# Performance work log

Measured on AMD Instinct MI355X. Metric: run time of the kernel, lower is better.

The kernel has to match this reference:

```python
import jax, jax.numpy as jnp
import numpy as np

B, S, D = 4, 2048, 1024
H, HD = 16, 64  # num_heads, head_dim
TD = H * HD     # total_dim
SCALE = HD ** -0.5


def setup_inputs() -> dict:
    key = jax.random.key(0)
    ks = jax.random.split(key, 9)
    std = 1.0 / np.sqrt(D)
    return {
        "x": jax.random.normal(ks[0], (B, S, D), dtype=jnp.float32),
        "Wq": jax.random.uniform(ks[1], (D, TD), jnp.float32, -std, std),
        "bq": jax.random.uniform(ks[2], (TD,), jnp.float32, -std, std),
        "Wk": jax.random.uniform(ks[3], (D, TD), jnp.float32, -std, std),
        "bk": jax.random.uniform(ks[4], (TD,), jnp.float32, -std, std),
        "Wv": jax.random.uniform(ks[5], (D, TD), jnp.float32, -std, std),
        "bv": jax.random.uniform(ks[6], (TD,), jnp.float32, -std, std),
        "Wo": jax.random.uniform(ks[7], (TD, D), jnp.float32, -std, std),
        "bo": jax.random.uniform(ks[8], (D,), jnp.float32, -std, std),
    }


def reference(x, Wq, bq, Wk, bk, Wv, bv, Wo, bo):
    # projections -> [B, H, S, HD]
    def split_heads(t):
        return t.reshape(B, S, H, HD).transpose(0, 2, 1, 3)

    q = split_heads(x @ Wq + bq)
    k = split_heads(x @ Wk + bk)
    v = split_heads(x @ Wv + bv)

    # attention scores [B, H, S, S]
    scores = jnp.einsum("bhqd,bhkd->bhqk", q, k) * SCALE
    weights = jax.nn.softmax(scores, axis=-1)
    # dropout is identity in eval mode (p effectively 0)
    attn = jnp.einsum("bhqk,bhkd->bhqd", weights, v)  # [B, H, S, HD]
    attn = attn.transpose(0, 2, 1, 3).reshape(B, S, TD)
    return attn @ Wo + bo
```

## Files before the change

### kernel.cpp

```cpp
#include <hip/hip_runtime.h>
#include <hip/hip_bf16.h>
#include <stdint.h>

#define B_ 4
#define S_ 2048
#define D_ 1024
#define H_ 16
#define HD_ 64
#define TD_ 1024

typedef __attribute__((ext_vector_type(4))) float f32x4;
typedef __attribute__((ext_vector_type(8))) __bf16 bf16x8;
typedef __attribute__((ext_vector_type(4))) __bf16 bf16x4;

__device__ __forceinline__ f32x4 mfma_16x16x32(bf16x8 a, bf16x8 b, f32x4 c) {
  return __builtin_amdgcn_mfma_f32_16x16x32_bf16(a, b, c, 0, 0, 0);
}

__device__ __forceinline__ float fexp2(float x) {
#if __has_builtin(__builtin_amdgcn_exp2f)
  return __builtin_amdgcn_exp2f(x);
#else
  return exp2f(x);
#endif
}

__device__ __forceinline__ uint32_t pkbf16(float lo, float hi) {
  uint32_t r;
  asm("v_cvt_pk_bf16_f32 %0, %1, %2" : "=v"(r) : "v"(lo), "v"(hi));
  return r;
}

__device__ __forceinline__ void gload16(const void* g, void* l) {
  __builtin_amdgcn_global_load_lds(
      (const __attribute__((address_space(1))) uint32_t*)(uintptr_t)g,
      (__attribute__((address_space(3))) uint32_t*)(uintptr_t)l,
      16, 0, 0);
}

__device__ __forceinline__ int xcd_swz(int flat, int nwg) {
  return (flat & 7) * (nwg >> 3) + (flat >> 3);
}


__global__ __launch_bounds__(256) void conv_x_kernel(const float* __restrict__ in,
                                                     __bf16* __restrict__ out) {
  size_t i = ((size_t)blockIdx.x * 256 + threadIdx.x) * 8;
  float4 a = *(const float4*)(in + i);
  float4 b = *(const float4*)(in + i + 4);
  bf16x8 o;
  o[0] = (__bf16)a.x; o[1] = (__bf16)a.y; o[2] = (__bf16)a.z; o[3] = (__bf16)a.w;
  o[4] = (__bf16)b.x; o[5] = (__bf16)b.y; o[6] = (__bf16)b.z; o[7] = (__bf16)b.w;
  *(bf16x8*)(out + i) = o;
}

__global__ __launch_bounds__(256) void wconv4_kernel(
    const float* __restrict__ w0, const float* __restrict__ w1,
    const float* __restrict__ w2, const float* __restrict__ w3,
    __bf16* __restrict__ o0, __bf16* __restrict__ o1,
    __bf16* __restrict__ o2, __bf16* __restrict__ o3, float scale0) {
  const float* in; __bf16* out; float scale;
  switch (blockIdx.z) {
    case 0: in = w0; out = o0; scale = scale0; break;
    case 1: in = w1; out = o1; scale = 1.0f; break;
    case 2: in = w2; out = o2; scale = 1.0f; break;
    default: in = w3; out = o3; scale = 1.0f; break;
  }
  __shared__ float t[64][65];
  const int bx = blockIdx.x * 64;
  const int by = blockIdx.y * 64;
  for (int e = threadIdx.x; e < 4096; e += 256) {
    int r = e >> 6, c = e & 63;
    t[r][c] = in[(size_t)(by + r) * 1024 + bx + c];
  }
  __syncthreads();
  for (int e = threadIdx.x; e < 4096; e += 256) {
    int r = e >> 6, c = e & 63;
    out[(size_t)(bx + r) * 1024 + by + c] = (__bf16)(t[c][r] * scale);
  }
}


#define STG3(SLOT)                                                      \
  gload16(srcA, dstA + (SLOT) * 8192);                                  \
  gload16(srcB, dstB + (SLOT) * 16384);                                 \
  gload16(srcB + 131072, dstB + (SLOT) * 16384 + 8192);                 \
  srcA += 32; srcB += 32;

#define COMPUTE_HALF(SLOT)                                              \
  {                                                                     \
    bf16x8 afr[4], bb[4];                                               \
    _Pragma("unroll") for (int mi = 0; mi < 4; ++mi)                    \
      afr[mi] = *(const bf16x8*)(aptr + (SLOT) * 8192 + mi * 1024);     \
    _Pragma("unroll") for (int ni = 0; ni < 4; ++ni)                    \
      bb[ni] = *(const bf16x8*)(bptr + (SLOT) * 16384 + ni * 1024);     \
    __builtin_amdgcn_s_setprio(1);                                      \
    _Pragma("unroll") for (int mi = 0; mi < 4; ++mi)                    \
      _Pragma("unroll") for (int ni = 0; ni < 4; ++ni)                  \
        acc[mi][ni] = mfma_16x16x32(afr[mi], bb[ni], acc[mi][ni]);      \
    __builtin_amdgcn_s_setprio(0);                                      \
  }

#define BAR_LGKM  asm volatile("s_waitcnt lgkmcnt(0)\n\ts_barrier" ::: "memory")
#define BAR_VM(N) asm volatile("s_waitcnt vmcnt(" #N ")\n\ts_barrier" ::: "memory")
#define BAR_VL(N) asm volatile("s_waitcnt vmcnt(" #N ") lgkmcnt(0)\n\ts_barrier" ::: "memory")

__global__ __launch_bounds__(512, 4) void gemm_qkv3(
    const __bf16* __restrict__ A, const __bf16* __restrict__ Bt,
    const float* __restrict__ bq, const float* __restrict__ bk,
    const float* __restrict__ bv, __bf16* __restrict__ Qout,
    __bf16* __restrict__ Kout, __bf16* __restrict__ Vout, float qscale) {
  __shared__ char SM[73728];
  const int tid = threadIdx.x, lane = tid & 63, wid = tid >> 6;
  const int lrow = lane & 15, g = lane >> 4;
  const int wm = wid >> 2, wn = wid & 3;
  const int flat = blockIdx.y * 12 + blockIdx.x;
  const int swz = xcd_swz(flat, 768);
  const int n0 = (swz % 12) * 256, m0 = (swz / 12) * 128;

  f32x4 acc[4][4];
  const f32x4 zero = {0.f, 0.f, 0.f, 0.f};
#pragma unroll
  for (int i = 0; i < 4; ++i)
#pragma unroll
    for (int j = 0; j < 4; ++j) acc[i][j] = zero;

  const int r0 = tid >> 2, c0 = tid & 3;
  const int csw = c0 ^ ((r0 >> 1) & 3);
  const __bf16* srcA = A + (size_t)(m0 + r0) * 1024 + csw * 8;
  const __bf16* srcB = Bt + (size_t)(n0 + r0) * 1024 + csw * 8;
  char* dstA = SM + wid * 1024;
  char* dstB = SM + 24576 + wid * 1024;

  const int sw = (lrow >> 1) & 3;
  const char* aptr = SM + (wm * 64 + lrow) * 64 + ((g ^ sw) << 4);
  const char* bptr = SM + 24576 + (wn * 64 + lrow) * 64 + ((g ^ sw) << 4);

  STG3(0)
  STG3(1)
  asm volatile("s_waitcnt vmcnt(3)\n\ts_barrier" ::: "memory");

  for (int it = 0; it < 10; ++it) {
    STG3(2)
    COMPUTE_HALF(0)
    BAR_VL(3);
    STG3(0)
    COMPUTE_HALF(1)
    BAR_VL(3);
    STG3(1)
    COMPUTE_HALF(2)
    BAR_VL(3);
  }
  COMPUTE_HALF(0)
  BAR_VL(0);
  COMPUTE_HALF(1)

  const int sel = n0 >> 10;
  if (sel < 2) {
    const float* bias = sel ? bk : bq;
    const float bsc = sel ? 1.0f : qscale;
    __bf16* Out = sel ? Kout : Qout;
#pragma unroll
    for (int mi = 0; mi < 4; ++mi) {
#pragma unroll
      for (int ni = 0; ni < 4; ++ni) {
        const int mbase = m0 + wm * 64 + mi * 16 + g * 4;
        const int nloc = (n0 & 1023) + wn * 64 + ni * 16 + lrow;
        const float bvc = bias[nloc] * bsc;
        const int h = nloc >> 6, hd = nloc & 63;
#pragma unroll
        for (int r = 0; r < 4; ++r) {
          const int m = mbase + r;
          const int b = m >> 11, s = m & 2047;
          Out[((size_t)(b * H_ + h) * S_ + s) * HD_ + hd] = (__bf16)(acc[mi][ni][r] + bvc);
        }
      }
    }
  } else {
#pragma unroll
    for (int mi = 0; mi < 4; ++mi) {
#pragma unroll
      for (int ni = 0; ni < 4; ++ni) {
        const int mbase = m0 + wm * 64 + mi * 16 + g * 4;
        const int t = (n0 & 1023) + wn * 64 + ni * 16 + lrow;
        const float bvc = bv[t];
        bf16x4 w;
#pragma unroll
        for (int r = 0; r < 4; ++r) w[r] = (__bf16)(acc[mi][ni][r] + bvc);
        *(bf16x4*)(Vout + (size_t)t * (B_ * S_) + mbase) = w;
      }
    }
  }
}


#define STG_O(SLOT, KOFF)                                               \
  gload16(srcA + (KOFF), dstA + (SLOT) * 8192);                         \
  gload16(srcA + 65536 + (KOFF), dstA + (SLOT) * 8192 + 4096);          \
  gload16(srcB + (KOFF), dstB + (SLOT) * 8192);                         \
  gload16(srcB + 65536 + (KOFF), dstB + (SLOT) * 8192 + 4096);

#define COMPUTE_O(SLOT)                                                 \
  {                                                                     \
    bf16x8 afr[4], bb[4];                                               \
    _Pragma("unroll") for (int mi = 0; mi < 4; ++mi)                    \
      afr[mi] = *(const bf16x8*)(aptr + (SLOT) * 8192 + mi * 1024);     \
    _Pragma("unroll") for (int ni = 0; ni < 4; ++ni)                    \
      bb[ni] = *(const bf16x8*)(bptr + (SLOT) * 8192 + ni * 1024);      \
    __builtin_amdgcn_s_setprio(1);                                      \
    _Pragma("unroll") for (int mi = 0; mi < 4; ++mi)                    \
      _Pragma("unroll") for (int ni = 0; ni < 4; ++ni)                  \
        acc[mi][ni] = mfma_16x16x32(afr[mi], bb[ni], acc[mi][ni]);      \
    __builtin_amdgcn_s_setprio(0);                                      \
  }

__global__ __launch_bounds__(256, 4) void gemm_out_ring(
    const __bf16* __restrict__ A, const __bf16* __restrict__ Bt,
    const float* __restrict__ bias, float* __restrict__ Cout) {
  __shared__ char SM[32768];
  const int tid = threadIdx.x, lane = tid & 63, wid = tid >> 6;
  const int lrow = lane & 15, g = lane >> 4;
  const int wm = wid >> 1, wn = wid & 1;
  const int flat = blockIdx.y * 8 + blockIdx.x;
  const int swz = xcd_swz(flat, 512);
  const int n0 = (swz & 7) * 128, m0 = (swz >> 3) * 128;

  f32x4 acc[4][4];
  const f32x4 zero = {0.f, 0.f, 0.f, 0.f};
#pragma unroll
  for (int i = 0; i < 4; ++i)
#pragma unroll
    for (int j = 0; j < 4; ++j) acc[i][j] = zero;

  const int r0 = tid >> 2, c0 = tid & 3;
  const int csw = c0 ^ ((r0 >> 1) & 3);
  const __bf16* srcA = A + (size_t)(m0 + r0) * 1024 + csw * 8;
  const __bf16* srcB = Bt + (size_t)(n0 + r0) * 1024 + csw * 8;
  char* dstA = SM + wid * 1024;
  char* dstB = SM + 16384 + wid * 1024;

  const int sw = (lrow >> 1) & 3;
  const char* aptr = SM + (wm * 64 + lrow) * 64 + ((g ^ sw) << 4);
  const char* bptr = SM + 16384 + (wn * 64 + lrow) * 64 + ((g ^ sw) << 4);

  STG_O(0, 0)
  STG_O(1, 32)
  srcA += 64; srcB += 64;
  BAR_VM(4);

  for (int it = 0; it < 15; ++it) {
    COMPUTE_O(0)
    BAR_LGKM;
    STG_O(0, 0)
    BAR_VM(4);
    COMPUTE_O(1)
    BAR_LGKM;
    STG_O(1, 32)
    BAR_VM(4);
    srcA += 64; srcB += 64;
  }
  COMPUTE_O(0)
  BAR_LGKM;
  BAR_VM(0);
  COMPUTE_O(1)

#pragma unroll
  for (int mi = 0; mi < 4; ++mi) {
#pragma unroll
    for (int ni = 0; ni < 4; ++ni) {
      const int mbase = m0 + wm * 64 + mi * 16 + g * 4;
      const int ncol = n0 + wn * 64 + ni * 16 + lrow;
      const float bvc = bias[ncol];
#pragma unroll
      for (int r = 0; r < 4; ++r)
        Cout[(size_t)(mbase + r) * 1024 + ncol] = acc[mi][ni][r] + bvc;
    }
  }
}


__global__ __launch_bounds__(256, 4) void attn_kernel(
    const __bf16* __restrict__ Q, const __bf16* __restrict__ Kp,
    const __bf16* __restrict__ VT, __bf16* __restrict__ O) {
  const int flat = blockIdx.y * gridDim.x + blockIdx.x;
  const int swz = (flat & 7) * 128 + (flat >> 3);
  const int bh = swz >> 4;
  const int q0 = (swz & 15) * 128;
  const int tid = threadIdx.x, lane = tid & 63, wid = tid >> 6;
  const int lrow = lane & 15, g = lane >> 4;
  const int s7 = lrow & 7;
  const int b = bh >> 4, h = bh & 15;

  const __bf16* Qb = Q + (size_t)bh * S_ * HD_;

  __shared__ char SMEM[32768];

  const int qrowA = q0 + wid * 32 + lrow;
  const int qrowB = qrowA + 16;
  const bf16x8 qf0a = *(const bf16x8*)(Qb + (size_t)qrowA * HD_ + g * 8);
  const bf16x8 qf1a = *(const bf16x8*)(Qb + (size_t)qrowA * HD_ + 32 + g * 8);
  const bf16x8 qf0b = *(const bf16x8*)(Qb + (size_t)qrowB * HD_ + g * 8);
  const bf16x8 qf1b = *(const bf16x8*)(Qb + (size_t)qrowB * HD_ + 32 + g * 8);

  bf16x8 ones;
#pragma unroll
  for (int i = 0; i < 8; ++i) ones[i] = (__bf16)1.0f;

  const int gi0 = wid * 64 + lane;
  const int row0 = gi0 >> 3, sg0 = gi0 & 7;
  const int kc0 = sg0 ^ (row0 & 7);
  const int kvoff = row0 * HD_ + kc0 * 8;
  const int vvoff = row0 * (B_ * S_) + kc0 * 8;
  const __bf16* Kt = Kp + (size_t)bh * S_ * HD_;
  const __bf16* Vt = VT + (size_t)(h * HD_) * (B_ * S_) + b * S_;
  char* kd0 = SMEM + wid * 1024;
  char* vd0 = SMEM + 16384 + wid * 1024;

  const char* addrA = SMEM + lrow * 128 + ((g ^ s7) << 4);
  const char* addrB = SMEM + lrow * 128 + (((4 + g) ^ s7) << 4);

  f32x4 laccA, laccB;
  f32x4 oaA[4], oaB[4];
  const f32x4 zero = {0.f, 0.f, 0.f, 0.f};
  const f32x4 minit = {-8.f, -8.f, -8.f, -8.f};
  laccA = zero; laccB = zero;
#pragma unroll
  for (int i = 0; i < 4; ++i) { oaA[i] = zero; oaB[i] = zero; }

  gload16(Kt + kvoff, kd0); gload16(Kt + 32 * HD_ + kvoff, kd0 + 4096);
  gload16(Vt + vvoff, vd0); gload16(Vt + (size_t)32 * (B_ * S_) + vvoff, vd0 + 4096);
  Kt += 64 * HD_; Vt += 64;
  __syncthreads();

  auto stage = [&](const int bo) {
    gload16(Kt + kvoff, kd0 + bo); gload16(Kt + 32 * HD_ + kvoff, kd0 + bo + 4096);
    gload16(Vt + vvoff, vd0 + bo);
    gload16(Vt + (size_t)32 * (B_ * S_) + vvoff, vd0 + bo + 4096);
    Kt += 64 * HD_; Vt += 64;
  };

  auto compute = [&](const int bo) {
    f32x4 sa[4], sb[4];
    __builtin_amdgcn_s_setprio(1);
#pragma unroll
    for (int kt = 0; kt < 4; ++kt) {
      bf16x8 kf0 = *(const bf16x8*)(addrA + bo + kt * 2048);
      bf16x8 kf1 = *(const bf16x8*)(addrB + bo + kt * 2048);
      f32x4 ca = minit;
      ca = mfma_16x16x32(kf0, qf0a, ca);
      ca = mfma_16x16x32(kf1, qf1a, ca);
      sa[kt] = ca;
      f32x4 cb = minit;
      cb = mfma_16x16x32(kf0, qf0b, cb);
      cb = mfma_16x16x32(kf1, qf1b, cb);
      sb[kt] = cb;
    }
    __builtin_amdgcn_s_setprio(0);

#pragma unroll
    for (int kt = 0; kt < 4; ++kt)
#pragma unroll
      for (int r = 0; r < 4; ++r) {
        sa[kt][r] = fexp2(sa[kt][r]);
        sb[kt][r] = fexp2(sb[kt][r]);
      }

    bf16x8 pfa[2], pfb[2];
#pragma unroll
    for (int s = 0; s < 2; ++s) {
      {
        uint32_t a0 = pkbf16(sa[2 * s][0], sa[2 * s][1]);
        uint32_t a1 = pkbf16(sa[2 * s][2], sa[2 * s][3]);
        uint32_t b0 = pkbf16(sa[2 * s + 1][0], sa[2 * s + 1][1]);
        uint32_t b1 = pkbf16(sa[2 * s + 1][2], sa[2 * s + 1][3]);
        asm volatile("v_permlane32_swap_b32 %0, %1" : "+v"(a0), "+v"(b0));
        asm volatile("v_permlane32_swap_b32 %0, %1" : "+v"(a1), "+v"(b1));
        asm volatile("v_permlane16_swap_b32 %0, %1" : "+v"(a0), "+v"(b0));
        asm volatile("v_permlane16_swap_b32 %0, %1" : "+v"(a1), "+v"(b1));
        union { uint32_t u[4]; bf16x8 v; } pu;
        pu.u[0] = a0; pu.u[1] = a1; pu.u[2] = b0; pu.u[3] = b1;
        pfa[s] = pu.v;
      }
      {
        uint32_t a0 = pkbf16(sb[2 * s][0], sb[2 * s][1]);
        uint32_t a1 = pkbf16(sb[2 * s][2], sb[2 * s][3]);
        uint32_t b0 = pkbf16(sb[2 * s + 1][0], sb[2 * s + 1][1]);
        uint32_t b1 = pkbf16(sb[2 * s + 1][2], sb[2 * s + 1][3]);
        asm volatile("v_permlane32_swap_b32 %0, %1" : "+v"(a0), "+v"(b0));
        asm volatile("v_permlane32_swap_b32 %0, %1" : "+v"(a1), "+v"(b1));
        asm volatile("v_permlane16_swap_b32 %0, %1" : "+v"(a0), "+v"(b0));
        asm volatile("v_permlane16_swap_b32 %0, %1" : "+v"(a1), "+v"(b1));
        union { uint32_t u[4]; bf16x8 v; } pu;
        pu.u[0] = a0; pu.u[1] = a1; pu.u[2] = b0; pu.u[3] = b1;
        pfb[s] = pu.v;
      }
    }

    __builtin_amdgcn_s_setprio(1);
#pragma unroll
    for (int band = 0; band < 4; ++band) {
      bf16x8 vf0 = *(const bf16x8*)(addrA + 16384 + bo + band * 2048);
      bf16x8 vf1 = *(const bf16x8*)(addrB + 16384 + bo + band * 2048);
      oaA[band] = mfma_16x16x32(vf0, pfa[0], oaA[band]);
      oaA[band] = mfma_16x16x32(vf1, pfa[1], oaA[band]);
      oaB[band] = mfma_16x16x32(vf0, pfb[0], oaB[band]);
      oaB[band] = mfma_16x16x32(vf1, pfb[1], oaB[band]);
    }
    laccA = mfma_16x16x32(ones, pfa[0], laccA);
    laccA = mfma_16x16x32(ones, pfa[1], laccA);
    laccB = mfma_16x16x32(ones, pfb[0], laccB);
    laccB = mfma_16x16x32(ones, pfb[1], laccB);
    __builtin_amdgcn_s_setprio(0);
  };

  for (int t = 0; t < S_ / 64; t += 2) {
    stage(8192);
    compute(0);
    __syncthreads();
    if (t + 2 < S_ / 64) stage(0);
    compute(8192);
    __syncthreads();
  }

  const float invA = 1.f / laccA[0];
  const float invB = 1.f / laccB[0];
  __bf16* opA = O + ((size_t)(b * S_ + qrowA)) * TD_ + h * HD_;
  __bf16* opB = O + ((size_t)(b * S_ + qrowB)) * TD_ + h * HD_;
#pragma unroll
  for (int band = 0; band < 4; ++band) {
    bf16x4 wa, wb;
#pragma unroll
    for (int r = 0; r < 4; ++r) {
      wa[r] = (__bf16)(oaA[band][r] * invA);
      wb[r] = (__bf16)(oaB[band][r] * invB);
    }
    *(bf16x4*)(opA + band * 16 + g * 4) = wa;
    *(bf16x4*)(opB + band * 16 + g * 4) = wb;
  }
}


extern "C" void kernel_launch(void* const* d_in, const int* in_sizes, int n_in,
                              void* d_out, int out_size, void* d_ws, size_t ws_size,
                              hipStream_t stream) {
  const float* x = (const float*)d_in[0];
  const float* Wq = (const float*)d_in[1];
  const float* bq = (const float*)d_in[2];
  const float* Wk = (const float*)d_in[3];
  const float* bk = (const float*)d_in[4];
  const float* Wv = (const float*)d_in[5];
  const float* bv = (const float*)d_in[6];
  const float* Wo = (const float*)d_in[7];
  const float* bo = (const float*)d_in[8];

  char* p = (char*)d_ws;
  const size_t SZ_X = (size_t)B_ * S_ * D_ * 2;
  const size_t SZ_W = (size_t)D_ * TD_ * 2;
  const size_t SZ_QKV = (size_t)B_ * H_ * S_ * HD_ * 2;
  __bf16* xb = (__bf16*)p;  p += SZ_X;
  __bf16* wqT = (__bf16*)p; p += SZ_W;
  __bf16* wkT = (__bf16*)p; p += SZ_W;
  __bf16* wvT = (__bf16*)p; p += SZ_W;
  __bf16* woT = (__bf16*)p; p += SZ_W;
  __bf16* Qb = (__bf16*)p;  p += SZ_QKV;
  __bf16* Kb = (__bf16*)p;  p += SZ_QKV;
  __bf16* VTb = (__bf16*)p; p += SZ_QKV;
  __bf16* attn = xb;

  const float SCALE_Q = 0.125f * 1.4426950408889634f;

  conv_x_kernel<<<4096, 256, 0, stream>>>(x, xb);
  wconv4_kernel<<<dim3(16, 16, 4), 256, 0, stream>>>(Wq, Wk, Wv, Wo,
                                                     wqT, wkT, wvT, woT, SCALE_Q);

  gemm_qkv3<<<dim3(12, 64), 512, 0, stream>>>(
      xb, wqT, bq, bk, bv, Qb, Kb, VTb, SCALE_Q);

  attn_kernel<<<dim3(16, 64), 256, 0, stream>>>(Qb, Kb, VTb, attn);

  gemm_out_ring<<<dim3(8, 64), 256, 0, stream>>>(attn, woT, bo, (float*)d_out);
}
```

Before: 172.4 us.

## Triple-buffer K/V tiles in attention kernel with vmcnt-based barriers

Extends LDS staging of K and V tiles from double to triple buffering, with two tiles prefetched ahead of compute. The main loop is restructured into a rotating three-slot schedule with partial vmcnt waits, so loads for a later tile stay in flight while the current tile is computed. This aims to hide global-memory latency better. In exchange, shared memory per block grows to 48 KB, which may reduce how many blocks fit on a CU.

```diff
diff --git a/kernel.cpp b/kernel.cpp
--- a/kernel.cpp
+++ b/kernel.cpp
@@ -293,7 +293,7 @@
 
   const __bf16* Qb = Q + (size_t)bh * S_ * HD_;
 
-  __shared__ char SMEM[32768];
+  __shared__ char SMEM[49152];
 
   const int qrowA = q0 + wid * 32 + lrow;
   const int qrowB = qrowA + 16;
@@ -314,7 +314,7 @@
   const __bf16* Kt = Kp + (size_t)bh * S_ * HD_;
   const __bf16* Vt = VT + (size_t)(h * HD_) * (B_ * S_) + b * S_;
   char* kd0 = SMEM + wid * 1024;
-  char* vd0 = SMEM + 16384 + wid * 1024;
+  char* vd0 = SMEM + 24576 + wid * 1024;
 
   const char* addrA = SMEM + lrow * 128 + ((g ^ s7) << 4);
   const char* addrB = SMEM + lrow * 128 + (((4 + g) ^ s7) << 4);
@@ -327,25 +327,21 @@
 #pragma unroll
   for (int i = 0; i < 4; ++i) { oaA[i] = zero; oaB[i] = zero; }
 
-  gload16(Kt + kvoff, kd0); gload16(Kt + 32 * HD_ + kvoff, kd0 + 4096);
-  gload16(Vt + vvoff, vd0); gload16(Vt + (size_t)32 * (B_ * S_) + vvoff, vd0 + 4096);
-  Kt += 64 * HD_; Vt += 64;
-  __syncthreads();
-
-  auto stage = [&](const int bo) {
-    gload16(Kt + kvoff, kd0 + bo); gload16(Kt + 32 * HD_ + kvoff, kd0 + bo + 4096);
-    gload16(Vt + vvoff, vd0 + bo);
-    gload16(Vt + (size_t)32 * (B_ * S_) + vvoff, vd0 + bo + 4096);
+  auto stage = [&](const int so) {
+    gload16(Kt + kvoff, kd0 + so);
+    gload16(Kt + 32 * HD_ + kvoff, kd0 + so + 4096);
+    gload16(Vt + vvoff, vd0 + so);
+    gload16(Vt + (size_t)32 * (B_ * S_) + vvoff, vd0 + so + 4096);
     Kt += 64 * HD_; Vt += 64;
   };
 
-  auto compute = [&](const int bo) {
+  auto compute = [&](const int so) {
     f32x4 sa[4], sb[4];
     __builtin_amdgcn_s_setprio(1);
 #pragma unroll
     for (int kt = 0; kt < 4; ++kt) {
-      bf16x8 kf0 = *(const bf16x8*)(addrA + bo + kt * 2048);
-      bf16x8 kf1 = *(const bf16x8*)(addrB + bo + kt * 2048);
+      bf16x8 kf0 = *(const bf16x8*)(addrA + so + kt * 2048);
+      bf16x8 kf1 = *(const bf16x8*)(addrB + so + kt * 2048);
       f32x4 ca = minit;
       ca = mfma_16x16x32(kf0, qf0a, ca);
       ca = mfma_16x16x32(kf1, qf1a, ca);
@@ -399,8 +395,8 @@
     __builtin_amdgcn_s_setprio(1);
 #pragma unroll
     for (int band = 0; band < 4; ++band) {
-      bf16x8 vf0 = *(const bf16x8*)(addrA + 16384 + bo + band * 2048);
-      bf16x8 vf1 = *(const bf16x8*)(addrB + 16384 + bo + band * 2048);
+      bf16x8 vf0 = *(const bf16x8*)(addrA + 24576 + so + band * 2048);
+      bf16x8 vf1 = *(const bf16x8*)(addrB + 24576 + so + band * 2048);
       oaA[band] = mfma_16x16x32(vf0, pfa[0], oaA[band]);
       oaA[band] = mfma_16x16x32(vf1, pfa[1], oaA[band]);
       oaB[band] = mfma_16x16x32(vf0, pfb[0], oaB[band]);
@@ -413,14 +409,18 @@
     __builtin_amdgcn_s_setprio(0);
   };
 
-  for (int t = 0; t < S_ / 64; t += 2) {
-    stage(8192);
-    compute(0);
-    __syncthreads();
-    if (t + 2 < S_ / 64) stage(0);
-    compute(8192);
-    __syncthreads();
-  }
+  stage(0);
+  stage(8192);
+  BAR_VM(4);
+
+  for (int it = 0; it < 10; ++it) {
+    stage(16384); compute(0);     BAR_VL(4);
+    stage(0);     compute(8192);  BAR_VL(4);
+    stage(8192);  compute(16384); BAR_VL(4);
+  }
+  compute(0);
+  BAR_VL(0);
+  compute(8192);
 
   const float invA = 1.f / laccA[0];
   const float invB = 1.f / laccB[0];
```

Result: slower. 181.3 us (+5.2%).
